# Kernel optimization log

Measured on AMD Instinct MI355X. Metric: run time of the kernel, lower is better.

The kernel has to match this reference:

```python
import jax, jax.numpy as jnp
import numpy as np
from jax import lax

B, H, W, C = 16, 256, 256, 1
LOC_C = 31            # channels out of localization network
BN_EPS = 1e-3         # Keras BatchNormalization default epsilon
NEG_SLOPE = 0.1       # LeakyReLU slope


def _conv_relu(x, k, b):
    y = lax.conv_general_dilated(x, k, (1, 1), 'SAME',
                                 dimension_numbers=('NHWC', 'HWIO', 'NHWC'))
    return jax.nn.relu(y + b)


def _maxpool2(x):
    return lax.reduce_window(x, -jnp.inf, lax.max, (1, 2, 2, 1), (1, 2, 2, 1), 'VALID')


def _resize_nearest(x, out_h, out_w):
    # tf.image.resize(..., method='nearest') with half-pixel centers
    b, h, w, c = x.shape
    ih = jnp.floor((jnp.arange(out_h) + 0.5) * h / out_h).astype(jnp.int32)
    iw = jnp.floor((jnp.arange(out_w) + 0.5) * w / out_w).astype(jnp.int32)
    return x[:, ih][:, :, iw]


def _generate_grid(theta, height, width):
    # base grid in [-1, 1], x varies along width, y along height
    xs = jnp.arange(width, dtype=jnp.float32) / (width - 1) * 2.0 - 1.0
    ys = jnp.arange(height, dtype=jnp.float32) / (height - 1) * 2.0 - 1.0
    gx, gy = jnp.meshgrid(xs, ys)                      # (H, W)
    grid = jnp.stack([gx, gy], axis=-1).reshape(height * width, 2)  # (HW, 2)
    th = theta.reshape(-1, 2, 3)
    A = th[:, :, :2]                                   # (B, 2, 2)
    t = th[:, :, 2]                                    # (B, 2)
    # NOTE: source does grid @ A (not A @ grid) -- replicate exactly
    tg = jnp.einsum('nc,bcd->bnd', grid, A) + t[:, None, :]
    return tg.reshape(-1, height, width, 2)


def _sampler(img, grid):
    b, h, w, c = img.shape
    x = 0.5 * ((grid[..., 0] + 1.0) * (w - 1))
    y = 0.5 * ((grid[..., 1] + 1.0) * (h - 1))
    x0 = jnp.floor(x); x1 = x0 + 1.0
    y0 = jnp.floor(y); y1 = y0 + 1.0
    x0 = jnp.clip(x0, 0.0, w - 1.0); x1 = jnp.clip(x1, 0.0, w - 1.0)
    y0 = jnp.clip(y0, 0.0, h - 1.0); y1 = jnp.clip(y1, 0.0, h - 1.0)
    wa = (x1 - x) * (y1 - y)
    wb = (x1 - x) * (y - y0)
    wc = (x - x0) * (y1 - y)
    wd = (x - x0) * (y - y0)
    xi0 = x0.astype(jnp.int32); xi1 = x1.astype(jnp.int32)
    yi0 = y0.astype(jnp.int32); yi1 = y1.astype(jnp.int32)
    img_flat = img.reshape(b, h * w, c)

    def gather(yi, xi):
        idx = (yi * w + xi).reshape(b, h * w, 1)       # (B, HW, 1)
        return jnp.take_along_axis(img_flat, idx, axis=1).reshape(b, h, w, c)

    Ia = gather(yi0, xi0)
    Ib = gather(yi1, xi0)
    Ic = gather(yi0, xi1)
    Id = gather(yi1, xi1)
    return (wa[..., None] * Ia + wb[..., None] * Ib
            + wc[..., None] * Ic + wd[..., None] * Id)


def setup_inputs() -> dict:
    key = jax.random.key(0)
    ks = jax.random.split(key, 16)
    s = 0.05
    feat = (H // 8) * (W // 8) * LOC_C  # 31744 flattened localization features
    return {
        'x': jax.random.normal(ks[0], (B, H, W, C), jnp.float32),
        'conv1_k': jax.random.normal(ks[1], (3, 3, C, 8), jnp.float32) * s,
        'conv1_b': jnp.zeros((8,), jnp.float32),
        'conv2_k': jax.random.normal(ks[2], (3, 3, 8, 16), jnp.float32) * s,
        'conv2_b': jnp.zeros((16,), jnp.float32),
        'conv3_k': jax.random.normal(ks[3], (3, 3, 16, LOC_C), jnp.float32) * s,
        'conv3_b': jnp.zeros((LOC_C,), jnp.float32),
        'bn_gamma': 1.0 + 0.1 * jax.random.normal(ks[4], (feat,), jnp.float32),
        'bn_beta': 0.1 * jax.random.normal(ks[5], (feat,), jnp.float32),
        'bn_mean': jnp.zeros((feat,), jnp.float32),
        'bn_var': jnp.ones((feat,), jnp.float32),
        'd1_k': jax.random.normal(ks[6], (feat, 64), jnp.float32) * 0.01,
        'd1_b': jnp.zeros((64,), jnp.float32),
        'd2_k': jax.random.normal(ks[7], (64, 96), jnp.float32) * s,
        'd2_b': jnp.zeros((96,), jnp.float32),
        'd3_k': jax.random.normal(ks[8], (96, 6), jnp.float32) * 0.01,
        'd3_b': jnp.array([1, 0, 0, 0, 1, 0], jnp.float32),
    }


def reference(x, conv1_k, conv1_b, conv2_k, conv2_b, conv3_k, conv3_b,
              bn_gamma, bn_beta, bn_mean, bn_var,
              d1_k, d1_b, d2_k, d2_b, d3_k, d3_b):
    # localization network: (conv-relu, pool) x3 -> (B, H/8, W/8, 31)
    xi = _maxpool2(_conv_relu(x, conv1_k, conv1_b))
    xi = _maxpool2(_conv_relu(xi, conv2_k, conv2_b))
    x_intermediate = _maxpool2(_conv_relu(xi, conv3_k, conv3_b))
    # transformation parameter network (BN in inference mode, dropout = identity)
    f = x_intermediate.reshape(x.shape[0], -1)
    f = (f - bn_mean) * jax.lax.rsqrt(bn_var + BN_EPS) * bn_gamma + bn_beta
    f = jax.nn.relu(f @ d1_k + d1_b)
    f = jax.nn.relu(f @ d2_k + d2_b)
    theta = f @ d3_k + d3_b                            # (B, 6)
    grid = _generate_grid(theta, H, W)                 # (B, H, W, 2)
    loc_up = _resize_nearest(x_intermediate, H, W)     # (B, H, W, 31)
    xc = jnp.concatenate([x, loc_up], axis=-1)         # (B, H, W, 32)
    out = _sampler(xc, grid)
    return jnp.where(out >= 0, out, NEG_SLOPE * out)
```

## Files before the change

### kernel.cpp

```cpp
#include <hip/hip_runtime.h>


#define NEG_SLOPE 0.1f
#define BN_EPS 1e-3f

typedef float vfloat4 __attribute__((ext_vector_type(4)));

__device__ __forceinline__ void fma4v(float pv, float4 wq, float* __restrict__ acc) {
    acc[0] = fmaf(pv, wq.x, acc[0]);
    acc[1] = fmaf(pv, wq.y, acc[1]);
    acc[2] = fmaf(pv, wq.z, acc[2]);
    acc[3] = fmaf(pv, wq.w, acc[3]);
}

__global__ __launch_bounds__(256) void st_conv1(const float* __restrict__ x,
                                                const float* __restrict__ w,
                                                const float* __restrict__ bias,
                                                float* __restrict__ Ap,
                                                float* __restrict__ Bp) {
    int idx = blockIdx.x * 256 + threadIdx.x;
    int px = idx & 127, py = (idx >> 7) & 127, b = idx >> 14;
    const float* xb = x + b * 65536;
    int iy0 = 2 * py - 1, ix0 = 2 * px - 1;
    float p[16];
#pragma unroll
    for (int r = 0; r < 4; ++r) {
        int iy = iy0 + r;
        bool oky = (iy >= 0) && (iy < 256);
#pragma unroll
        for (int cc = 0; cc < 4; ++cc) {
            int ix = ix0 + cc;
            bool ok = oky && (ix >= 0) && (ix < 256);
            p[r * 4 + cc] = ok ? xb[iy * 256 + ix] : 0.0f;
        }
    }
    float m[8];
#pragma unroll
    for (int co = 0; co < 8; ++co) m[co] = -1e30f;
#pragma unroll
    for (int oy = 0; oy < 2; ++oy)
#pragma unroll
        for (int ox = 0; ox < 2; ++ox) {
            float acc[8];
#pragma unroll
            for (int co = 0; co < 8; ++co) acc[co] = 0.0f;
#pragma unroll
            for (int ky = 0; ky < 3; ++ky)
#pragma unroll
                for (int kx = 0; kx < 3; ++kx) {
                    float pv = p[(oy + ky) * 4 + (ox + kx)];
                    const float* wr = w + (ky * 3 + kx) * 8;
#pragma unroll
                    for (int co = 0; co < 8; ++co)
                        acc[co] = fmaf(pv, wr[co], acc[co]);
                }
#pragma unroll
            for (int co = 0; co < 8; ++co) m[co] = fmaxf(m[co], acc[co]);
        }
    float4 o0, o1;
    float r0 = m[0] + bias[0], r1 = m[1] + bias[1], r2 = m[2] + bias[2], r3 = m[3] + bias[3];
    float r4 = m[4] + bias[4], r5 = m[5] + bias[5], r6 = m[6] + bias[6], r7 = m[7] + bias[7];
    o0.x = r0 > 0.f ? r0 : 0.f; o0.y = r1 > 0.f ? r1 : 0.f;
    o0.z = r2 > 0.f ? r2 : 0.f; o0.w = r3 > 0.f ? r3 : 0.f;
    o1.x = r4 > 0.f ? r4 : 0.f; o1.y = r5 > 0.f ? r5 : 0.f;
    o1.z = r6 > 0.f ? r6 : 0.f; o1.w = r7 > 0.f ? r7 : 0.f;
    float* o = Ap + ((b * 130 + py + 1) * 130 + (px + 1)) * 8;
    *(float4*)o = o0;
    *(float4*)(o + 4) = o1;

    const float4 z4 = {0.f, 0.f, 0.f, 0.f};
    if (idx < 8256) {
        int bb = idx / 516, t = idx - bb * 516;
        int iy, ix;
        if (t < 130)      { iy = 0;       ix = t; }
        else if (t < 260) { iy = 129;     ix = t - 130; }
        else if (t < 388) { iy = t - 259; ix = 0; }
        else              { iy = t - 387; ix = 129; }
        float* d = Ap + ((bb * 130 + iy) * 130 + ix) * 8;
        *(float4*)d = z4; *(float4*)(d + 4) = z4;
    } else if (idx < 12416) {
        int r = idx - 8256;
        int bb = r / 260, t = r - bb * 260;
        int iy, ix;
        if (t < 66)       { iy = 0;       ix = t; }
        else if (t < 132) { iy = 65;      ix = t - 66; }
        else if (t < 196) { iy = t - 131; ix = 0; }
        else              { iy = t - 195; ix = 65; }
        float* d = Bp + ((bb * 66 + iy) * 66 + ix) * 16;
        *(float4*)d = z4; *(float4*)(d + 4) = z4;
        *(float4*)(d + 8) = z4; *(float4*)(d + 12) = z4;
    }
}

__global__ __launch_bounds__(256) void st_conv2(const float* __restrict__ Ap,
                                                const float* __restrict__ w,
                                                const float* __restrict__ bias,
                                                float* __restrict__ Bp) {
    __shared__ __align__(16) float wlds[1152];
    int t = threadIdx.x;
    for (int i = t; i < 1152; i += 256) wlds[i] = w[i];
    __syncthreads();
    int lane = t & 63;
    int wv = __builtin_amdgcn_readfirstlane(t >> 6);
    int cobase = wv * 4;
    int pixel = blockIdx.x * 64 + lane;
    int px = pixel & 63, py = (pixel >> 6) & 63, b = pixel >> 12;
    const float* Ab = Ap + b * 135200;
    int rowbase = (2 * py) * 130 + 2 * px;
    float acc[4][4];
#pragma unroll
    for (int pos = 0; pos < 4; ++pos)
#pragma unroll
        for (int c = 0; c < 4; ++c) acc[pos][c] = 0.0f;

#pragma unroll
    for (int ciq = 0; ciq < 2; ++ciq) {
        float ps[64];
#pragma unroll
        for (int r = 0; r < 4; ++r)
#pragma unroll
            for (int cc = 0; cc < 4; ++cc) {
                float4 v = *(const float4*)(Ab + (rowbase + r * 130 + cc) * 8 + ciq * 4);
                int cell = r * 4 + cc;
                ps[cell * 4 + 0] = v.x; ps[cell * 4 + 1] = v.y;
                ps[cell * 4 + 2] = v.z; ps[cell * 4 + 3] = v.w;
            }
#pragma unroll
        for (int ky = 0; ky < 3; ++ky)
#pragma unroll
            for (int kx = 0; kx < 3; ++kx) {
                int tap = ky * 3 + kx;
#pragma unroll
                for (int comp = 0; comp < 4; ++comp) {
                    float4 wq = *(const float4*)&wlds[((tap * 8 + ciq * 4 + comp) << 4) + cobase];
#pragma unroll
                    for (int oy = 0; oy < 2; ++oy)
#pragma unroll
                        for (int ox = 0; ox < 2; ++ox) {
                            float pv = ps[((oy + ky) * 4 + (ox + kx)) * 4 + comp];
                            fma4v(pv, wq, acc[oy * 2 + ox]);
                        }
                }
            }
    }
    float4 o;
    float* oc = (float*)&o;
#pragma unroll
    for (int c = 0; c < 4; ++c) {
        float m = fmaxf(fmaxf(acc[0][c], acc[1][c]), fmaxf(acc[2][c], acc[3][c]));
        m += bias[cobase + c];
        oc[c] = m > 0.0f ? m : 0.0f;
    }
    *(float4*)(Bp + ((b * 66 + py + 1) * 66 + (px + 1)) * 16 + cobase) = o;
}

__global__ __launch_bounds__(256) void st_conv3(const float* __restrict__ Bp,
                                                const float* __restrict__ w,
                                                const float* __restrict__ bias,
                                                float* __restrict__ xip) {
    __shared__ __align__(16) float wlds[9 * 16 * 32];
    int t = threadIdx.x;
    for (int i = t; i < 4464; i += 256) {
        int tapci = i / 31;
        int co = i - tapci * 31;
        wlds[(tapci << 5) + co] = w[i];
    }
    __syncthreads();
    int lane = t & 63;
    int wv = __builtin_amdgcn_readfirstlane(t >> 6);
    int quad = blockIdx.y * 4 + wv;
    int cobase = quad * 4;
    if (cobase > 27) cobase = 27;
    int pixel = blockIdx.x * 64 + lane;
    int b = pixel >> 10;
    int cell = pixel & 1023;
    int ppy = cell >> 5, ppx = cell & 31;
    const float* Bb = Bp + b * 69696;
    int rowbase = (2 * ppy) * 66 + 2 * ppx;
    float acc[4][4];
#pragma unroll
    for (int pos = 0; pos < 4; ++pos)
#pragma unroll
        for (int c = 0; c < 4; ++c) acc[pos][c] = 0.0f;

#pragma unroll 2
    for (int ciq = 0; ciq < 4; ++ciq) {
        float ps[64];
#pragma unroll
        for (int r = 0; r < 4; ++r)
#pragma unroll
            for (int cc = 0; cc < 4; ++cc) {
                float4 v = *(const float4*)(Bb + (rowbase + r * 66 + cc) * 16 + ciq * 4);
                int cell2 = r * 4 + cc;
                ps[cell2 * 4 + 0] = v.x; ps[cell2 * 4 + 1] = v.y;
                ps[cell2 * 4 + 2] = v.z; ps[cell2 * 4 + 3] = v.w;
            }
#pragma unroll
        for (int ky = 0; ky < 3; ++ky)
#pragma unroll
            for (int kx = 0; kx < 3; ++kx) {
                int tap = ky * 3 + kx;
#pragma unroll
                for (int comp = 0; comp < 4; ++comp) {
                    float4 wq = *(const float4*)&wlds[((tap * 16 + ciq * 4 + comp) << 5) + cobase];
#pragma unroll
                    for (int oy = 0; oy < 2; ++oy)
#pragma unroll
                        for (int ox = 0; ox < 2; ++ox) {
                            float pv = ps[((oy + ky) * 4 + (ox + kx)) * 4 + comp];
                            fma4v(pv, wq, acc[oy * 2 + ox]);
                        }
                }
            }
    }
    float* xcell = xip + (b << 15) + (cell << 5) + 1 + cobase;
#pragma unroll
    for (int c = 0; c < 4; ++c) {
        float m = fmaxf(fmaxf(acc[0][c], acc[1][c]), fmaxf(acc[2][c], acc[3][c]));
        m += bias[cobase + c];
        xcell[c] = m > 0.0f ? m : 0.0f;
    }
}

__global__ __launch_bounds__(256) void st_d1(const float* __restrict__ xip,
                                             const float* __restrict__ gamma,
                                             const float* __restrict__ beta,
                                             const float* __restrict__ mean,
                                             const float* __restrict__ var,
                                             const float* __restrict__ k1,
                                             float* __restrict__ partial) {
    int t = threadIdx.x, s = blockIdx.x;
    int o = t & 63;
    int sub = t >> 6;
    int subu = __builtin_amdgcn_readfirstlane(sub);
    int j0 = s * 64 + subu * 16;
    float acc[16];
#pragma unroll
    for (int b = 0; b < 16; ++b) acc[b] = 0.0f;
#pragma unroll 4
    for (int jj = 0; jj < 16; ++jj) {
        int j = j0 + jj;
        float kv = k1[j * 64 + o];
        int cell = j / 31;
        int co = j - cell * 31;
        const float* xj = xip + (cell << 5) + 1 + co;
        float sc = gamma[j] * rsqrtf(var[j] + BN_EPS);
        float mn = mean[j], bt = beta[j];
#pragma unroll
        for (int b = 0; b < 16; ++b) {
            float v = xj[b << 15];
            float f = (v - mn) * sc + bt;
            acc[b] = fmaf(f, kv, acc[b]);
        }
    }
    __shared__ float red[4][16][64];
#pragma unroll
    for (int b = 0; b < 16; ++b) red[sub][b][o] = acc[b];
    __syncthreads();
    if (sub == 0) {
#pragma unroll
        for (int b = 0; b < 16; ++b) {
            float v = red[0][b][o] + red[1][b][o] + red[2][b][o] + red[3][b][o];
            partial[b * 31744 + s * 64 + o] = v;
        }
    }
}

__global__ __launch_bounds__(256) void st_head(const float* __restrict__ partial,
                                               const float* __restrict__ b1,
                                               const float* __restrict__ k2,
                                               const float* __restrict__ b2,
                                               const float* __restrict__ k3,
                                               const float* __restrict__ b3,
                                               float* __restrict__ theta) {
    int b = blockIdx.x, t = threadIdx.x;
    __shared__ float red[4][64];
    __shared__ float h1[64];
    __shared__ float h2[96];
    int o = t & 63, qq = t >> 6;
    const float* pb = partial + b * 31744;
    float s = 0.0f;
    int sl0 = qq * 124;
#pragma unroll 4
    for (int sl = sl0; sl < sl0 + 124; ++sl)
        s += pb[sl * 64 + o];
    red[qq][o] = s;
    __syncthreads();
    if (t < 64) {
        float v = red[0][t] + red[1][t] + red[2][t] + red[3][t] + b1[t];
        h1[t] = v > 0.0f ? v : 0.0f;
    }
    __syncthreads();
    if (t < 96) {
        float v = b2[t];
        for (int i = 0; i < 64; ++i) v = fmaf(h1[i], k2[i * 96 + t], v);
        h2[t] = v > 0.0f ? v : 0.0f;
    }
    __syncthreads();
    if (t < 6) {
        float v = b3[t];
        for (int i = 0; i < 96; ++i) v = fmaf(h2[i], k3[i * 6 + t], v);
        theta[b * 6 + t] = v;
    }
}

__global__ __launch_bounds__(256) void st_sample(const float* __restrict__ x,
                                                 const float* __restrict__ xip,
                                                 const float* __restrict__ theta,
                                                 float* __restrict__ out) {
    int gid = blockIdx.x * 256 + threadIdx.x;
    int q = gid & 3;
    int pix = gid >> 2;
    int ow = pix & 255, oh = (pix >> 8) & 255;
    int b = __builtin_amdgcn_readfirstlane(blockIdx.x >> 10);

    const float* th = theta + b * 6;
    float t0 = th[0], t1 = th[1], t2 = th[2], t3 = th[3], t4 = th[4], t5 = th[5];
    float gx = (float)ow * (2.0f / 255.0f) - 1.0f;
    float gy = (float)oh * (2.0f / 255.0f) - 1.0f;
    float sx = gx * t0 + gy * t3 + t2;
    float sy = gx * t1 + gy * t4 + t5;
    float xf = 0.5f * ((sx + 1.0f) * 255.0f);
    float yf = 0.5f * ((sy + 1.0f) * 255.0f);
    float x0 = floorf(xf), y0 = floorf(yf);
    float x1 = x0 + 1.0f, y1 = y0 + 1.0f;
    x0 = fminf(fmaxf(x0, 0.0f), 255.0f);
    x1 = fminf(fmaxf(x1, 0.0f), 255.0f);
    y0 = fminf(fmaxf(y0, 0.0f), 255.0f);
    y1 = fminf(fmaxf(y1, 0.0f), 255.0f);
    float wa = (x1 - xf) * (y1 - yf);
    float wb = (x1 - xf) * (yf - y0);
    float wc = (xf - x0) * (y1 - yf);
    float wd = (xf - x0) * (yf - y0);
    int xi0 = (int)x0, xi1 = (int)x1, yi0 = (int)y0, yi1 = (int)y1;

    const float* cellbase = xip + (b << 15);
    int off = q * 8;
    const float* pa = cellbase + ((((yi0 >> 3) << 5) + (xi0 >> 3)) << 5) + off;
    const float* pb = cellbase + ((((yi1 >> 3) << 5) + (xi0 >> 3)) << 5) + off;
    const float* pc = cellbase + ((((yi0 >> 3) << 5) + (xi1 >> 3)) << 5) + off;
    const float* pd = cellbase + ((((yi1 >> 3) << 5) + (xi1 >> 3)) << 5) + off;

    float r[8];
#pragma unroll
    for (int k = 0; k < 2; ++k) {
        float4 va = *(const float4*)(pa + 4 * k);
        float4 vb = *(const float4*)(pb + 4 * k);
        float4 vc = *(const float4*)(pc + 4 * k);
        float4 vd = *(const float4*)(pd + 4 * k);
        r[4 * k]     = fmaf(wa, va.x, fmaf(wb, vb.x, fmaf(wc, vc.x, wd * vd.x)));
        r[4 * k + 1] = fmaf(wa, va.y, fmaf(wb, vb.y, fmaf(wc, vc.y, wd * vd.y)));
        r[4 * k + 2] = fmaf(wa, va.z, fmaf(wb, vb.z, fmaf(wc, vc.z, wd * vd.z)));
        r[4 * k + 3] = fmaf(wa, va.w, fmaf(wb, vb.w, fmaf(wc, vc.w, wd * vd.w)));
    }
    if (q == 0) {
        const float* xb = x + b * 65536;
        float Ia = xb[yi0 * 256 + xi0];
        float Ib = xb[yi1 * 256 + xi0];
        float Ic = xb[yi0 * 256 + xi1];
        float Id = xb[yi1 * 256 + xi1];
        r[0] = fmaf(wa, Ia, fmaf(wb, Ib, fmaf(wc, Ic, wd * Id)));
    }
#pragma unroll
    for (int i = 0; i < 8; ++i) r[i] = r[i] >= 0.0f ? r[i] : NEG_SLOPE * r[i];

    float* ob = out + pix * 32 + off;
    vfloat4 v0 = {r[0], r[1], r[2], r[3]};
    vfloat4 v1 = {r[4], r[5], r[6], r[7]};
    __builtin_nontemporal_store(v0, (vfloat4*)ob);
    __builtin_nontemporal_store(v1, (vfloat4*)(ob + 4));
}

extern "C" void kernel_launch(void* const* d_in, const int* in_sizes, int n_in,
                              void* d_out, int out_size, void* d_ws, size_t ws_size,
                              hipStream_t stream) {
    const float* x     = (const float*)d_in[0];
    const float* c1k   = (const float*)d_in[1];
    const float* c1b   = (const float*)d_in[2];
    const float* c2k   = (const float*)d_in[3];
    const float* c2b   = (const float*)d_in[4];
    const float* c3k   = (const float*)d_in[5];
    const float* c3b   = (const float*)d_in[6];
    const float* gamma = (const float*)d_in[7];
    const float* beta  = (const float*)d_in[8];
    const float* mean  = (const float*)d_in[9];
    const float* var   = (const float*)d_in[10];
    const float* d1k   = (const float*)d_in[11];
    const float* d1b   = (const float*)d_in[12];
    const float* d2k   = (const float*)d_in[13];
    const float* d2b   = (const float*)d_in[14];
    const float* d3k   = (const float*)d_in[15];
    const float* d3b   = (const float*)d_in[16];
    float* out = (float*)d_out;
    float* ws  = (float*)d_ws;

    float* Ap      = ws;
    float* Bp      = ws + 2163200;
    float* xip     = ws;
    float* partial = ws + 3278336;
    float* theta   = ws + 3786240;

    st_conv1<<<1024, 256, 0, stream>>>(x, c1k, c1b, Ap, Bp);
    st_conv2<<<1024, 256, 0, stream>>>(Ap, c2k, c2b, Bp);
    st_conv3<<<dim3(256, 2), 256, 0, stream>>>(Bp, c3k, c3b, xip);
    st_d1<<<496, 256, 0, stream>>>(xip, gamma, beta, mean, var, d1k, partial);
    st_head<<<16, 256, 0, stream>>>(partial, d1b, d2k, d2b, d3k, d3b, theta);
    st_sample<<<16384, 256, 0, stream>>>(x, xip, theta, out);
}
```

Baseline: 257.1 us.

## Fuse all six stages into one persistent kernel with grid barriers

Replaces the six separate launches (conv1, conv2, conv3, dense-1 partials, head, sampler) with a single persistent kernel of 512 blocks. Stages are separated by a software grid barrier built on an atomic counter and generation word, and each block loops over the work that used to be spread across many blocks. The aim is to remove per-launch overhead and the idle gaps between kernels. In exchange it depends on all 512 blocks being resident at once, which the barrier needs to avoid deadlock, and the sampler runs with fewer blocks looping, which may reduce latency hiding.

```diff
diff --git a/kernel.cpp b/kernel.cpp
--- a/kernel.cpp
+++ b/kernel.cpp
@@ -3,6 +3,7 @@
 
 #define NEG_SLOPE 0.1f
 #define BN_EPS 1e-3f
+#define NBLOCKS 512u
 
 typedef float vfloat4 __attribute__((ext_vector_type(4)));
 
@@ -13,362 +14,382 @@
     acc[3] = fmaf(pv, wq.w, acc[3]);
 }
 
-__global__ __launch_bounds__(256) void st_conv1(const float* __restrict__ x,
-                                                const float* __restrict__ w,
-                                                const float* __restrict__ bias,
-                                                float* __restrict__ Ap,
-                                                float* __restrict__ Bp) {
-    int idx = blockIdx.x * 256 + threadIdx.x;
-    int px = idx & 127, py = (idx >> 7) & 127, b = idx >> 14;
-    const float* xb = x + b * 65536;
-    int iy0 = 2 * py - 1, ix0 = 2 * px - 1;
-    float p[16];
-#pragma unroll
-    for (int r = 0; r < 4; ++r) {
-        int iy = iy0 + r;
-        bool oky = (iy >= 0) && (iy < 256);
-#pragma unroll
-        for (int cc = 0; cc < 4; ++cc) {
-            int ix = ix0 + cc;
-            bool ok = oky && (ix >= 0) && (ix < 256);
-            p[r * 4 + cc] = ok ? xb[iy * 256 + ix] : 0.0f;
-        }
-    }
-    float m[8];
-#pragma unroll
-    for (int co = 0; co < 8; ++co) m[co] = -1e30f;
-#pragma unroll
-    for (int oy = 0; oy < 2; ++oy)
-#pragma unroll
-        for (int ox = 0; ox < 2; ++ox) {
-            float acc[8];
-#pragma unroll
-            for (int co = 0; co < 8; ++co) acc[co] = 0.0f;
+__device__ __forceinline__ void grid_barrier(unsigned* counter, unsigned* gen) {
+    __syncthreads();
+    if (threadIdx.x == 0) {
+        __threadfence();
+        unsigned g = __hip_atomic_load(gen, __ATOMIC_RELAXED, __HIP_MEMORY_SCOPE_AGENT);
+        unsigned arrived = __hip_atomic_fetch_add(counter, 1u, __ATOMIC_ACQ_REL,
+                                                  __HIP_MEMORY_SCOPE_AGENT);
+        if (arrived == NBLOCKS - 1u) {
+            __hip_atomic_store(counter, 0u, __ATOMIC_RELAXED, __HIP_MEMORY_SCOPE_AGENT);
+            __hip_atomic_store(gen, g + 1u, __ATOMIC_RELEASE, __HIP_MEMORY_SCOPE_AGENT);
+        } else {
+            while (__hip_atomic_load(gen, __ATOMIC_ACQUIRE, __HIP_MEMORY_SCOPE_AGENT) == g) {
+                __builtin_amdgcn_s_sleep(8);
+            }
+        }
+        __threadfence();
+    }
+    __syncthreads();
+}
+
+__global__ __launch_bounds__(256, 2) void st_mega(
+    const float* __restrict__ x,
+    const float* __restrict__ c1k, const float* __restrict__ c1b,
+    const float* __restrict__ c2k, const float* __restrict__ c2b,
+    const float* __restrict__ c3k, const float* __restrict__ c3b,
+    const float* __restrict__ gamma, const float* __restrict__ beta,
+    const float* __restrict__ mean, const float* __restrict__ var,
+    const float* __restrict__ d1k, const float* __restrict__ d1b,
+    const float* __restrict__ d2k, const float* __restrict__ d2b,
+    const float* __restrict__ d3k, const float* __restrict__ d3b,
+    float* __restrict__ Ap, float* __restrict__ Bp,
+    float* __restrict__ partial, float* __restrict__ theta,
+    unsigned* __restrict__ barC, unsigned* __restrict__ barG,
+    float* __restrict__ out)
+{
+    __shared__ __align__(16) float smem[4608];
+    const int t = threadIdx.x;
+    const int bid = blockIdx.x;
+    const int gtid = bid * 256 + t;
+    const int lane = t & 63;
+    float* xip = Ap;
+
+#pragma unroll
+    for (int it = 0; it < 2; ++it) {
+        int idx = it * 131072 + gtid;
+        int px = idx & 127, py = (idx >> 7) & 127, b = idx >> 14;
+        const float* xb = x + b * 65536;
+        int iy0 = 2 * py - 1, ix0 = 2 * px - 1;
+        float p[16];
+#pragma unroll
+        for (int r = 0; r < 4; ++r) {
+            int iy = iy0 + r;
+            bool oky = (iy >= 0) && (iy < 256);
+#pragma unroll
+            for (int cc = 0; cc < 4; ++cc) {
+                int ix = ix0 + cc;
+                bool ok = oky && (ix >= 0) && (ix < 256);
+                p[r * 4 + cc] = ok ? xb[iy * 256 + ix] : 0.0f;
+            }
+        }
+        float m[8];
+#pragma unroll
+        for (int co = 0; co < 8; ++co) m[co] = -1e30f;
+#pragma unroll
+        for (int oy = 0; oy < 2; ++oy)
+#pragma unroll
+            for (int ox = 0; ox < 2; ++ox) {
+                float acc[8];
+#pragma unroll
+                for (int co = 0; co < 8; ++co) acc[co] = 0.0f;
+#pragma unroll
+                for (int ky = 0; ky < 3; ++ky)
+#pragma unroll
+                    for (int kx = 0; kx < 3; ++kx) {
+                        float pv = p[(oy + ky) * 4 + (ox + kx)];
+                        const float* wr = c1k + (ky * 3 + kx) * 8;
+#pragma unroll
+                        for (int co = 0; co < 8; ++co)
+                            acc[co] = fmaf(pv, wr[co], acc[co]);
+                    }
+#pragma unroll
+                for (int co = 0; co < 8; ++co) m[co] = fmaxf(m[co], acc[co]);
+            }
+        float4 o0, o1;
+        float r0 = m[0] + c1b[0], r1 = m[1] + c1b[1], r2 = m[2] + c1b[2], r3 = m[3] + c1b[3];
+        float r4 = m[4] + c1b[4], r5 = m[5] + c1b[5], r6 = m[6] + c1b[6], r7 = m[7] + c1b[7];
+        o0.x = r0 > 0.f ? r0 : 0.f; o0.y = r1 > 0.f ? r1 : 0.f;
+        o0.z = r2 > 0.f ? r2 : 0.f; o0.w = r3 > 0.f ? r3 : 0.f;
+        o1.x = r4 > 0.f ? r4 : 0.f; o1.y = r5 > 0.f ? r5 : 0.f;
+        o1.z = r6 > 0.f ? r6 : 0.f; o1.w = r7 > 0.f ? r7 : 0.f;
+        float* o = Ap + ((b * 130 + py + 1) * 130 + (px + 1)) * 8;
+        *(float4*)o = o0;
+        *(float4*)(o + 4) = o1;
+
+        const float4 z4 = {0.f, 0.f, 0.f, 0.f};
+        if (idx < 8256) {
+            int bb = idx / 516, tt = idx - bb * 516;
+            int iy, ix;
+            if (tt < 130)      { iy = 0;        ix = tt; }
+            else if (tt < 260) { iy = 129;      ix = tt - 130; }
+            else if (tt < 388) { iy = tt - 259; ix = 0; }
+            else               { iy = tt - 387; ix = 129; }
+            float* d = Ap + ((bb * 130 + iy) * 130 + ix) * 8;
+            *(float4*)d = z4; *(float4*)(d + 4) = z4;
+        } else if (idx < 12416) {
+            int r = idx - 8256;
+            int bb = r / 260, tt = r - bb * 260;
+            int iy, ix;
+            if (tt < 66)       { iy = 0;        ix = tt; }
+            else if (tt < 132) { iy = 65;       ix = tt - 66; }
+            else if (tt < 196) { iy = tt - 131; ix = 0; }
+            else               { iy = tt - 195; ix = 65; }
+            float* d = Bp + ((bb * 66 + iy) * 66 + ix) * 16;
+            *(float4*)d = z4; *(float4*)(d + 4) = z4;
+            *(float4*)(d + 8) = z4; *(float4*)(d + 12) = z4;
+        }
+    }
+    grid_barrier(barC, barG);
+
+    {
+        for (int i = t; i < 1152; i += 256) smem[i] = c2k[i];
+        __syncthreads();
+        int wv = __builtin_amdgcn_readfirstlane(t >> 6);
+        int cobase = wv * 4;
+#pragma unroll
+        for (int it = 0; it < 2; ++it) {
+            int pixel = (it * 512 + bid) * 64 + lane;
+            int px = pixel & 63, py = (pixel >> 6) & 63, b = pixel >> 12;
+            const float* Ab = Ap + b * 135200;
+            int rowbase = (2 * py) * 130 + 2 * px;
+            float acc[4][4];
+#pragma unroll
+            for (int pos = 0; pos < 4; ++pos)
+#pragma unroll
+                for (int c = 0; c < 4; ++c) acc[pos][c] = 0.0f;
+#pragma unroll
+            for (int ciq = 0; ciq < 2; ++ciq) {
+                float ps[64];
+#pragma unroll
+                for (int r = 0; r < 4; ++r)
+#pragma unroll
+                    for (int cc = 0; cc < 4; ++cc) {
+                        float4 v = *(const float4*)(Ab + (rowbase + r * 130 + cc) * 8 + ciq * 4);
+                        int cell = r * 4 + cc;
+                        ps[cell * 4 + 0] = v.x; ps[cell * 4 + 1] = v.y;
+                        ps[cell * 4 + 2] = v.z; ps[cell * 4 + 3] = v.w;
+                    }
+#pragma unroll
+                for (int ky = 0; ky < 3; ++ky)
+#pragma unroll
+                    for (int kx = 0; kx < 3; ++kx) {
+                        int tap = ky * 3 + kx;
+#pragma unroll
+                        for (int comp = 0; comp < 4; ++comp) {
+                            float4 wq = *(const float4*)&smem[((tap * 8 + ciq * 4 + comp) << 4) + cobase];
+#pragma unroll
+                            for (int oy = 0; oy < 2; ++oy)
+#pragma unroll
+                                for (int ox = 0; ox < 2; ++ox) {
+                                    float pv = ps[((oy + ky) * 4 + (ox + kx)) * 4 + comp];
+                                    fma4v(pv, wq, acc[oy * 2 + ox]);
+                                }
+                        }
+                    }
+            }
+            float4 o;
+            float* oc = (float*)&o;
+#pragma unroll
+            for (int c = 0; c < 4; ++c) {
+                float m = fmaxf(fmaxf(acc[0][c], acc[1][c]), fmaxf(acc[2][c], acc[3][c]));
+                m += c2b[cobase + c];
+                oc[c] = m > 0.0f ? m : 0.0f;
+            }
+            *(float4*)(Bp + ((b * 66 + py + 1) * 66 + (px + 1)) * 16 + cobase) = o;
+        }
+    }
+    grid_barrier(barC, barG);
+
+    {
+        for (int i = t; i < 4464; i += 256) {
+            int tapci = i / 31;
+            int co = i - tapci * 31;
+            smem[(tapci << 5) + co] = c3k[i];
+        }
+        __syncthreads();
+        int wv = __builtin_amdgcn_readfirstlane(t >> 6);
+        int quad = ((bid & 1) << 2) + wv;
+        int cobase = quad * 4;
+        if (cobase > 27) cobase = 27;
+        int pixel = (bid >> 1) * 64 + lane;
+        int b = pixel >> 10;
+        int cell = pixel & 1023;
+        int ppy = cell >> 5, ppx = cell & 31;
+        const float* Bb = Bp + b * 69696;
+        int rowbase = (2 * ppy) * 66 + 2 * ppx;
+        float acc[4][4];
+#pragma unroll
+        for (int pos = 0; pos < 4; ++pos)
+#pragma unroll
+            for (int c = 0; c < 4; ++c) acc[pos][c] = 0.0f;
+#pragma unroll 2
+        for (int ciq = 0; ciq < 4; ++ciq) {
+            float ps[64];
+#pragma unroll
+            for (int r = 0; r < 4; ++r)
+#pragma unroll
+                for (int cc = 0; cc < 4; ++cc) {
+                    float4 v = *(const float4*)(Bb + (rowbase + r * 66 + cc) * 16 + ciq * 4);
+                    int cell2 = r * 4 + cc;
+                    ps[cell2 * 4 + 0] = v.x; ps[cell2 * 4 + 1] = v.y;
+                    ps[cell2 * 4 + 2] = v.z; ps[cell2 * 4 + 3] = v.w;
+                }
 #pragma unroll
             for (int ky = 0; ky < 3; ++ky)
 #pragma unroll
                 for (int kx = 0; kx < 3; ++kx) {
-                    float pv = p[(oy + ky) * 4 + (ox + kx)];
-                    const float* wr = w + (ky * 3 + kx) * 8;
-#pragma unroll
-                    for (int co = 0; co < 8; ++co)
-                        acc[co] = fmaf(pv, wr[co], acc[co]);
+                    int tap = ky * 3 + kx;
+#pragma unroll
+                    for (int comp = 0; comp < 4; ++comp) {
+                        float4 wq = *(const float4*)&smem[((tap * 16 + ciq * 4 + comp) << 5) + cobase];
+#pragma unroll
+                        for (int oy = 0; oy < 2; ++oy)
+#pragma unroll
+                            for (int ox = 0; ox < 2; ++ox) {
+                                float pv = ps[((oy + ky) * 4 + (ox + kx)) * 4 + comp];
+                                fma4v(pv, wq, acc[oy * 2 + ox]);
+                            }
+                    }
                 }
-#pragma unroll
-            for (int co = 0; co < 8; ++co) m[co] = fmaxf(m[co], acc[co]);
-        }
-    float4 o0, o1;
-    float r0 = m[0] + bias[0], r1 = m[1] + bias[1], r2 = m[2] + bias[2], r3 = m[3] + bias[3];
-    float r4 = m[4] + bias[4], r5 = m[5] + bias[5], r6 = m[6] + bias[6], r7 = m[7] + bias[7];
-    o0.x = r0 > 0.f ? r0 : 0.f; o0.y = r1 > 0.f ? r1 : 0.f;
-    o0.z = r2 > 0.f ? r2 : 0.f; o0.w = r3 > 0.f ? r3 : 0.f;
-    o1.x = r4 > 0.f ? r4 : 0.f; o1.y = r5 > 0.f ? r5 : 0.f;
-    o1.z = r6 > 0.f ? r6 : 0.f; o1.w = r7 > 0.f ? r7 : 0.f;
-    float* o = Ap + ((b * 130 + py + 1) * 130 + (px + 1)) * 8;
-    *(float4*)o = o0;
-    *(float4*)(o + 4) = o1;
-
-    const float4 z4 = {0.f, 0.f, 0.f, 0.f};
-    if (idx < 8256) {
-        int bb = idx / 516, t = idx - bb * 516;
-        int iy, ix;
-        if (t < 130)      { iy = 0;       ix = t; }
-        else if (t < 260) { iy = 129;     ix = t - 130; }
-        else if (t < 388) { iy = t - 259; ix = 0; }
-        else              { iy = t - 387; ix = 129; }
-        float* d = Ap + ((bb * 130 + iy) * 130 + ix) * 8;
-        *(float4*)d = z4; *(float4*)(d + 4) = z4;
-    } else if (idx < 12416) {
-        int r = idx - 8256;
-        int bb = r / 260, t = r - bb * 260;
-        int iy, ix;
-        if (t < 66)       { iy = 0;       ix = t; }
-        else if (t < 132) { iy = 65;      ix = t - 66; }
-        else if (t < 196) { iy = t - 131; ix = 0; }
-        else              { iy = t - 195; ix = 65; }
-        float* d = Bp + ((bb * 66 + iy) * 66 + ix) * 16;
-        *(float4*)d = z4; *(float4*)(d + 4) = z4;
-        *(float4*)(d + 8) = z4; *(float4*)(d + 12) = z4;
-    }
-}
-
-__global__ __launch_bounds__(256) void st_conv2(const float* __restrict__ Ap,
-                                                const float* __restrict__ w,
-                                                const float* __restrict__ bias,
-                                                float* __restrict__ Bp) {
-    __shared__ __align__(16) float wlds[1152];
-    int t = threadIdx.x;
-    for (int i = t; i < 1152; i += 256) wlds[i] = w[i];
-    __syncthreads();
-    int lane = t & 63;
-    int wv = __builtin_amdgcn_readfirstlane(t >> 6);
-    int cobase = wv * 4;
-    int pixel = blockIdx.x * 64 + lane;
-    int px = pixel & 63, py = (pixel >> 6) & 63, b = pixel >> 12;
-    const float* Ab = Ap + b * 135200;
-    int rowbase = (2 * py) * 130 + 2 * px;
-    float acc[4][4];
-#pragma unroll
-    for (int pos = 0; pos < 4; ++pos)
-#pragma unroll
-        for (int c = 0; c < 4; ++c) acc[pos][c] = 0.0f;
-
-#pragma unroll
-    for (int ciq = 0; ciq < 2; ++ciq) {
-        float ps[64];
-#pragma unroll
-        for (int r = 0; r < 4; ++r)
-#pragma unroll
-            for (int cc = 0; cc < 4; ++cc) {
-                float4 v = *(const float4*)(Ab + (rowbase + r * 130 + cc) * 8 + ciq * 4);
-                int cell = r * 4 + cc;
-                ps[cell * 4 + 0] = v.x; ps[cell * 4 + 1] = v.y;
-                ps[cell * 4 + 2] = v.z; ps[cell * 4 + 3] = v.w;
-            }
-#pragma unroll
-        for (int ky = 0; ky < 3; ++ky)
-#pragma unroll
-            for (int kx = 0; kx < 3; ++kx) {
-                int tap = ky * 3 + kx;
-#pragma unroll
-                for (int comp = 0; comp < 4; ++comp) {
-                    float4 wq = *(const float4*)&wlds[((tap * 8 + ciq * 4 + comp) << 4) + cobase];
-#pragma unroll
-                    for (int oy = 0; oy < 2; ++oy)
-#pragma unroll
-                        for (int ox = 0; ox < 2; ++ox) {
-                            float pv = ps[((oy + ky) * 4 + (ox + kx)) * 4 + comp];
-                            fma4v(pv, wq, acc[oy * 2 + ox]);
-                        }
-                }
-            }
-    }
-    float4 o;
-    float* oc = (float*)&o;
-#pragma unroll
-    for (int c = 0; c < 4; ++c) {
-        float m = fmaxf(fmaxf(acc[0][c], acc[1][c]), fmaxf(acc[2][c], acc[3][c]));
-        m += bias[cobase + c];
-        oc[c] = m > 0.0f ? m : 0.0f;
-    }
-    *(float4*)(Bp + ((b * 66 + py + 1) * 66 + (px + 1)) * 16 + cobase) = o;
-}
-
-__global__ __launch_bounds__(256) void st_conv3(const float* __restrict__ Bp,
-                                                const float* __restrict__ w,
-                                                const float* __restrict__ bias,
-                                                float* __restrict__ xip) {
-    __shared__ __align__(16) float wlds[9 * 16 * 32];
-    int t = threadIdx.x;
-    for (int i = t; i < 4464; i += 256) {
-        int tapci = i / 31;
-        int co = i - tapci * 31;
-        wlds[(tapci << 5) + co] = w[i];
-    }
-    __syncthreads();
-    int lane = t & 63;
-    int wv = __builtin_amdgcn_readfirstlane(t >> 6);
-    int quad = blockIdx.y * 4 + wv;
-    int cobase = quad * 4;
-    if (cobase > 27) cobase = 27;
-    int pixel = blockIdx.x * 64 + lane;
-    int b = pixel >> 10;
-    int cell = pixel & 1023;
-    int ppy = cell >> 5, ppx = cell & 31;
-    const float* Bb = Bp + b * 69696;
-    int rowbase = (2 * ppy) * 66 + 2 * ppx;
-    float acc[4][4];
-#pragma unroll
-    for (int pos = 0; pos < 4; ++pos)
-#pragma unroll
-        for (int c = 0; c < 4; ++c) acc[pos][c] = 0.0f;
-
-#pragma unroll 2
-    for (int ciq = 0; ciq < 4; ++ciq) {
-        float ps[64];
-#pragma unroll
-        for (int r = 0; r < 4; ++r)
-#pragma unroll
-            for (int cc = 0; cc < 4; ++cc) {
-                float4 v = *(const float4*)(Bb + (rowbase + r * 66 + cc) * 16 + ciq * 4);
-                int cell2 = r * 4 + cc;
-                ps[cell2 * 4 + 0] = v.x; ps[cell2 * 4 + 1] = v.y;
-                ps[cell2 * 4 + 2] = v.z; ps[cell2 * 4 + 3] = v.w;
-            }
-#pragma unroll
-        for (int ky = 0; ky < 3; ++ky)
-#pragma unroll
-            for (int kx = 0; kx < 3; ++kx) {
-                int tap = ky * 3 + kx;
-#pragma unroll
-                for (int comp = 0; comp < 4; ++comp) {
-                    float4 wq = *(const float4*)&wlds[((tap * 16 + ciq * 4 + comp) << 5) + cobase];
-#pragma unroll
-                    for (int oy = 0; oy < 2; ++oy)
-#pragma unroll
-                        for (int ox = 0; ox < 2; ++ox) {
-                            float pv = ps[((oy + ky) * 4 + (ox + kx)) * 4 + comp];
-                            fma4v(pv, wq, acc[oy * 2 + ox]);
-                        }
-                }
-            }
-    }
-    float* xcell = xip + (b << 15) + (cell << 5) + 1 + cobase;
-#pragma unroll
-    for (int c = 0; c < 4; ++c) {
-        float m = fmaxf(fmaxf(acc[0][c], acc[1][c]), fmaxf(acc[2][c], acc[3][c]));
-        m += bias[cobase + c];
-        xcell[c] = m > 0.0f ? m : 0.0f;
-    }
-}
-
-__global__ __launch_bounds__(256) void st_d1(const float* __restrict__ xip,
-                                             const float* __restrict__ gamma,
-                                             const float* __restrict__ beta,
-                                             const float* __restrict__ mean,
-                                             const float* __restrict__ var,
-                                             const float* __restrict__ k1,
-                                             float* __restrict__ partial) {
-    int t = threadIdx.x, s = blockIdx.x;
-    int o = t & 63;
-    int sub = t >> 6;
-    int subu = __builtin_amdgcn_readfirstlane(sub);
-    int j0 = s * 64 + subu * 16;
-    float acc[16];
-#pragma unroll
-    for (int b = 0; b < 16; ++b) acc[b] = 0.0f;
+        }
+        float* xcell = xip + (b << 15) + (cell << 5) + 1 + cobase;
+#pragma unroll
+        for (int c = 0; c < 4; ++c) {
+            float m = fmaxf(fmaxf(acc[0][c], acc[1][c]), fmaxf(acc[2][c], acc[3][c]));
+            m += c3b[cobase + c];
+            xcell[c] = m > 0.0f ? m : 0.0f;
+        }
+    }
+    grid_barrier(barC, barG);
+
+    if (bid < 496) {
+        int s = bid;
+        int o = lane;
+        int sub = t >> 6;
+        int subu = __builtin_amdgcn_readfirstlane(sub);
+        int j0 = s * 64 + subu * 16;
+        float acc[16];
+#pragma unroll
+        for (int b = 0; b < 16; ++b) acc[b] = 0.0f;
 #pragma unroll 4
-    for (int jj = 0; jj < 16; ++jj) {
-        int j = j0 + jj;
-        float kv = k1[j * 64 + o];
-        int cell = j / 31;
-        int co = j - cell * 31;
-        const float* xj = xip + (cell << 5) + 1 + co;
-        float sc = gamma[j] * rsqrtf(var[j] + BN_EPS);
-        float mn = mean[j], bt = beta[j];
-#pragma unroll
-        for (int b = 0; b < 16; ++b) {
-            float v = xj[b << 15];
-            float f = (v - mn) * sc + bt;
-            acc[b] = fmaf(f, kv, acc[b]);
-        }
-    }
-    __shared__ float red[4][16][64];
-#pragma unroll
-    for (int b = 0; b < 16; ++b) red[sub][b][o] = acc[b];
-    __syncthreads();
-    if (sub == 0) {
-#pragma unroll
-        for (int b = 0; b < 16; ++b) {
-            float v = red[0][b][o] + red[1][b][o] + red[2][b][o] + red[3][b][o];
-            partial[b * 31744 + s * 64 + o] = v;
-        }
-    }
-}
-
-__global__ __launch_bounds__(256) void st_head(const float* __restrict__ partial,
-                                               const float* __restrict__ b1,
-                                               const float* __restrict__ k2,
-                                               const float* __restrict__ b2,
-                                               const float* __restrict__ k3,
-                                               const float* __restrict__ b3,
-                                               float* __restrict__ theta) {
-    int b = blockIdx.x, t = threadIdx.x;
-    __shared__ float red[4][64];
-    __shared__ float h1[64];
-    __shared__ float h2[96];
-    int o = t & 63, qq = t >> 6;
-    const float* pb = partial + b * 31744;
-    float s = 0.0f;
-    int sl0 = qq * 124;
+        for (int jj = 0; jj < 16; ++jj) {
+            int j = j0 + jj;
+            float kv = d1k[j * 64 + o];
+            int cell = j / 31;
+            int co = j - cell * 31;
+            const float* xj = xip + (cell << 5) + 1 + co;
+            float sc = gamma[j] * rsqrtf(var[j] + BN_EPS);
+            float mn = mean[j], bt = beta[j];
+#pragma unroll
+            for (int b = 0; b < 16; ++b) {
+                float v = xj[b << 15];
+                float f = (v - mn) * sc + bt;
+                acc[b] = fmaf(f, kv, acc[b]);
+            }
+        }
+        float (*red)[16][64] = (float (*)[16][64])smem;
+#pragma unroll
+        for (int b = 0; b < 16; ++b) red[sub][b][o] = acc[b];
+        __syncthreads();
+        if (sub == 0) {
+#pragma unroll
+            for (int b = 0; b < 16; ++b) {
+                float v = red[0][b][o] + red[1][b][o] + red[2][b][o] + red[3][b][o];
+                partial[b * 31744 + s * 64 + o] = v;
+            }
+        }
+    }
+    grid_barrier(barC, barG);
+
+    if (bid < 16) {
+        int b = bid;
+        float* redh = smem;
+        float* h1   = smem + 256;
+        float* h2   = smem + 320;
+        int o = lane, qq = t >> 6;
+        const float* pb = partial + b * 31744;
+        float s = 0.0f;
+        int sl0 = qq * 124;
 #pragma unroll 4
-    for (int sl = sl0; sl < sl0 + 124; ++sl)
-        s += pb[sl * 64 + o];
-    red[qq][o] = s;
-    __syncthreads();
-    if (t < 64) {
-        float v = red[0][t] + red[1][t] + red[2][t] + red[3][t] + b1[t];
-        h1[t] = v > 0.0f ? v : 0.0f;
-    }
-    __syncthreads();
-    if (t < 96) {
-        float v = b2[t];
-        for (int i = 0; i < 64; ++i) v = fmaf(h1[i], k2[i * 96 + t], v);
-        h2[t] = v > 0.0f ? v : 0.0f;
-    }
-    __syncthreads();
-    if (t < 6) {
-        float v = b3[t];
-        for (int i = 0; i < 96; ++i) v = fmaf(h2[i], k3[i * 6 + t], v);
-        theta[b * 6 + t] = v;
-    }
-}
-
-__global__ __launch_bounds__(256) void st_sample(const float* __restrict__ x,
-                                                 const float* __restrict__ xip,
-                                                 const float* __restrict__ theta,
-                                                 float* __restrict__ out) {
-    int gid = blockIdx.x * 256 + threadIdx.x;
-    int q = gid & 3;
-    int pix = gid >> 2;
-    int ow = pix & 255, oh = (pix >> 8) & 255;
-    int b = __builtin_amdgcn_readfirstlane(blockIdx.x >> 10);
-
-    const float* th = theta + b * 6;
-    float t0 = th[0], t1 = th[1], t2 = th[2], t3 = th[3], t4 = th[4], t5 = th[5];
-    float gx = (float)ow * (2.0f / 255.0f) - 1.0f;
-    float gy = (float)oh * (2.0f / 255.0f) - 1.0f;
-    float sx = gx * t0 + gy * t3 + t2;
-    float sy = gx * t1 + gy * t4 + t5;
-    float xf = 0.5f * ((sx + 1.0f) * 255.0f);
-    float yf = 0.5f * ((sy + 1.0f) * 255.0f);
-    float x0 = floorf(xf), y0 = floorf(yf);
-    float x1 = x0 + 1.0f, y1 = y0 + 1.0f;
-    x0 = fminf(fmaxf(x0, 0.0f), 255.0f);
-    x1 = fminf(fmaxf(x1, 0.0f), 255.0f);
-    y0 = fminf(fmaxf(y0, 0.0f), 255.0f);
-    y1 = fminf(fmaxf(y1, 0.0f), 255.0f);
-    float wa = (x1 - xf) * (y1 - yf);
-    float wb = (x1 - xf) * (yf - y0);
-    float wc = (xf - x0) * (y1 - yf);
-    float wd = (xf - x0) * (yf - y0);
-    int xi0 = (int)x0, xi1 = (int)x1, yi0 = (int)y0, yi1 = (int)y1;
-
-    const float* cellbase = xip + (b << 15);
-    int off = q * 8;
-    const float* pa = cellbase + ((((yi0 >> 3) << 5) + (xi0 >> 3)) << 5) + off;
-    const float* pb = cellbase + ((((yi1 >> 3) << 5) + (xi0 >> 3)) << 5) + off;
-    const float* pc = cellbase + ((((yi0 >> 3) << 5) + (xi1 >> 3)) << 5) + off;
-    const float* pd = cellbase + ((((yi1 >> 3) << 5) + (xi1 >> 3)) << 5) + off;
-
-    float r[8];
-#pragma unroll
-    for (int k = 0; k < 2; ++k) {
-        float4 va = *(const float4*)(pa + 4 * k);
-        float4 vb = *(const float4*)(pb + 4 * k);
-        float4 vc = *(const float4*)(pc + 4 * k);
-        float4 vd = *(const float4*)(pd + 4 * k);
-        r[4 * k]     = fmaf(wa, va.x, fmaf(wb, vb.x, fmaf(wc, vc.x, wd * vd.x)));
-        r[4 * k + 1] = fmaf(wa, va.y, fmaf(wb, vb.y, fmaf(wc, vc.y, wd * vd.y)));
-        r[4 * k + 2] = fmaf(wa, va.z, fmaf(wb, vb.z, fmaf(wc, vc.z, wd * vd.z)));
-        r[4 * k + 3] = fmaf(wa, va.w, fmaf(wb, vb.w, fmaf(wc, vc.w, wd * vd.w)));
-    }
-    if (q == 0) {
-        const float* xb = x + b * 65536;
-        float Ia = xb[yi0 * 256 + xi0];
-        float Ib = xb[yi1 * 256 + xi0];
-        float Ic = xb[yi0 * 256 + xi1];
-        float Id = xb[yi1 * 256 + xi1];
-        r[0] = fmaf(wa, Ia, fmaf(wb, Ib, fmaf(wc, Ic, wd * Id)));
-    }
-#pragma unroll
-    for (int i = 0; i < 8; ++i) r[i] = r[i] >= 0.0f ? r[i] : NEG_SLOPE * r[i];
-
-    float* ob = out + pix * 32 + off;
-    vfloat4 v0 = {r[0], r[1], r[2], r[3]};
-    vfloat4 v1 = {r[4], r[5], r[6], r[7]};
-    __builtin_nontemporal_store(v0, (vfloat4*)ob);
-    __builtin_nontemporal_store(v1, (vfloat4*)(ob + 4));
+        for (int sl = sl0; sl < sl0 + 124; ++sl)
+            s += pb[sl * 64 + o];
+        redh[qq * 64 + o] = s;
+        __syncthreads();
+        if (t < 64) {
+            float v = redh[t] + redh[64 + t] + redh[128 + t] + redh[192 + t] + d1b[t];
+            h1[t] = v > 0.0f ? v : 0.0f;
+        }
+        __syncthreads();
+        if (t < 96) {
+            float v = d2b[t];
+            for (int i = 0; i < 64; ++i) v = fmaf(h1[i], d2k[i * 96 + t], v);
+            h2[t] = v > 0.0f ? v : 0.0f;
+        }
+        __syncthreads();
+        if (t < 6) {
+            float v = d3b[t];
+            for (int i = 0; i < 96; ++i) v = fmaf(h2[i], d3k[i * 6 + t], v);
+            theta[b * 6 + t] = v;
+        }
+    }
+    grid_barrier(barC, barG);
+
+#pragma unroll 1
+    for (int it = 0; it < 32; ++it) {
+        int id = it * 131072 + gtid;
+        int q = id & 3;
+        int pix = id >> 2;
+        int ow = pix & 255, oh = (pix >> 8) & 255;
+        int b = it >> 1;
+
+        const float* th = theta + b * 6;
+        float t0 = th[0], t1 = th[1], t2 = th[2], t3 = th[3], t4 = th[4], t5 = th[5];
+        float gx = (float)ow * (2.0f / 255.0f) - 1.0f;
+        float gy = (float)oh * (2.0f / 255.0f) - 1.0f;
+        float sx = gx * t0 + gy * t3 + t2;
+        float sy = gx * t1 + gy * t4 + t5;
+        float xf = 0.5f * ((sx + 1.0f) * 255.0f);
+        float yf = 0.5f * ((sy + 1.0f) * 255.0f);
+        float x0 = floorf(xf), y0 = floorf(yf);
+        float x1 = x0 + 1.0f, y1 = y0 + 1.0f;
+        x0 = fminf(fmaxf(x0, 0.0f), 255.0f);
+        x1 = fminf(fmaxf(x1, 0.0f), 255.0f);
+        y0 = fminf(fmaxf(y0, 0.0f), 255.0f);
+        y1 = fminf(fmaxf(y1, 0.0f), 255.0f);
+        float wa = (x1 - xf) * (y1 - yf);
+        float wb = (x1 - xf) * (yf - y0);
+        float wc = (xf - x0) * (y1 - yf);
+        float wd = (xf - x0) * (yf - y0);
+        int xi0 = (int)x0, xi1 = (int)x1, yi0 = (int)y0, yi1 = (int)y1;
+
+        const float* cellbase = xip + (b << 15);
+        int off = q * 8;
+        const float* pa = cellbase + ((((yi0 >> 3) << 5) + (xi0 >> 3)) << 5) + off;
+        const float* pbp = cellbase + ((((yi1 >> 3) << 5) + (xi0 >> 3)) << 5) + off;
+        const float* pc = cellbase + ((((yi0 >> 3) << 5) + (xi1 >> 3)) << 5) + off;
+        const float* pd = cellbase + ((((yi1 >> 3) << 5) + (xi1 >> 3)) << 5) + off;
+
+        float r[8];
+#pragma unroll
+        for (int k = 0; k < 2; ++k) {
+            float4 va = *(const float4*)(pa + 4 * k);
+            float4 vb = *(const float4*)(pbp + 4 * k);
+            float4 vc = *(const float4*)(pc + 4 * k);
+            float4 vd = *(const float4*)(pd + 4 * k);
+            r[4 * k]     = fmaf(wa, va.x, fmaf(wb, vb.x, fmaf(wc, vc.x, wd * vd.x)));
+            r[4 * k + 1] = fmaf(wa, va.y, fmaf(wb, vb.y, fmaf(wc, vc.y, wd * vd.y)));
+            r[4 * k + 2] = fmaf(wa, va.z, fmaf(wb, vb.z, fmaf(wc, vc.z, wd * vd.z)));
+            r[4 * k + 3] = fmaf(wa, va.w, fmaf(wb, vb.w, fmaf(wc, vc.w, wd * vd.w)));
+        }
+        if (q == 0) {
+            const float* xb = x + b * 65536;
+            float Ia = xb[yi0 * 256 + xi0];
+            float Ib = xb[yi1 * 256 + xi0];
+            float Ic = xb[yi0 * 256 + xi1];
+            float Id = xb[yi1 * 256 + xi1];
+            r[0] = fmaf(wa, Ia, fmaf(wb, Ib, fmaf(wc, Ic, wd * Id)));
+        }
+#pragma unroll
+        for (int i = 0; i < 8; ++i) r[i] = r[i] >= 0.0f ? r[i] : NEG_SLOPE * r[i];
+
+        float* ob = out + pix * 32 + off;
+        vfloat4 v0 = {r[0], r[1], r[2], r[3]};
+        vfloat4 v1 = {r[4], r[5], r[6], r[7]};
+        __builtin_nontemporal_store(v0, (vfloat4*)ob);
+        __builtin_nontemporal_store(v1, (vfloat4*)(ob + 4));
+    }
 }
 
 extern "C" void kernel_launch(void* const* d_in, const int* in_sizes, int n_in,
@@ -396,14 +417,15 @@
 
     float* Ap      = ws;
     float* Bp      = ws + 2163200;
-    float* xip     = ws;
     float* partial = ws + 3278336;
     float* theta   = ws + 3786240;
-
-    st_conv1<<<1024, 256, 0, stream>>>(x, c1k, c1b, Ap, Bp);
-    st_conv2<<<1024, 256, 0, stream>>>(Ap, c2k, c2b, Bp);
-    st_conv3<<<dim3(256, 2), 256, 0, stream>>>(Bp, c3k, c3b, xip);
-    st_d1<<<496, 256, 0, stream>>>(xip, gamma, beta, mean, var, d1k, partial);
-    st_head<<<16, 256, 0, stream>>>(partial, d1b, d2k, d2b, d3k, d3b, theta);
-    st_sample<<<16384, 256, 0, stream>>>(x, xip, theta, out);
+    unsigned* barC = (unsigned*)(ws + 3786368);
+    unsigned* barG = (unsigned*)(ws + 3786384);
+
+    hipMemsetAsync((void*)barC, 0, 128, stream);
+
+    st_mega<<<NBLOCKS, 256, 0, stream>>>(
+        x, c1k, c1b, c2k, c2b, c3k, c3b, gamma, beta, mean, var,
+        d1k, d1b, d2k, d2b, d3k, d3b, Ap, Bp, partial, theta,
+        barC, barG, out);
 }
```

Result: slower. 924.5 us (+259.5%).

## Fuse conv1 and conv2 into one kernel with conv1 tile in LDS

Applied to the files above, without the earlier changes.

Merges the first conv+pool stage into the second conv kernel. Each block computes the four padded conv1 rows it needs into shared memory, then runs conv2 from LDS instead of a global intermediate buffer. This drops one launch and the global write and read of the 130x130x8 intermediate. In exchange, adjacent blocks recompute the overlapping conv1 halo row, and each block uses about 21 KB of LDS, which may lower occupancy.

```diff
diff --git a/kernel.cpp b/kernel.cpp
--- a/kernel.cpp
+++ b/kernel.cpp
@@ -13,100 +13,81 @@
     acc[3] = fmaf(pv, wq.w, acc[3]);
 }
 
-__global__ __launch_bounds__(256) void st_conv1(const float* __restrict__ x,
-                                                const float* __restrict__ w,
-                                                const float* __restrict__ bias,
-                                                float* __restrict__ Ap,
-                                                float* __restrict__ Bp) {
-    int idx = blockIdx.x * 256 + threadIdx.x;
-    int px = idx & 127, py = (idx >> 7) & 127, b = idx >> 14;
-    const float* xb = x + b * 65536;
-    int iy0 = 2 * py - 1, ix0 = 2 * px - 1;
-    float p[16];
-#pragma unroll
-    for (int r = 0; r < 4; ++r) {
-        int iy = iy0 + r;
-        bool oky = (iy >= 0) && (iy < 256);
-#pragma unroll
-        for (int cc = 0; cc < 4; ++cc) {
-            int ix = ix0 + cc;
-            bool ok = oky && (ix >= 0) && (ix < 256);
-            p[r * 4 + cc] = ok ? xb[iy * 256 + ix] : 0.0f;
-        }
-    }
-    float m[8];
-#pragma unroll
-    for (int co = 0; co < 8; ++co) m[co] = -1e30f;
-#pragma unroll
-    for (int oy = 0; oy < 2; ++oy)
-#pragma unroll
-        for (int ox = 0; ox < 2; ++ox) {
-            float acc[8];
-#pragma unroll
-            for (int co = 0; co < 8; ++co) acc[co] = 0.0f;
-#pragma unroll
-            for (int ky = 0; ky < 3; ++ky)
-#pragma unroll
-                for (int kx = 0; kx < 3; ++kx) {
-                    float pv = p[(oy + ky) * 4 + (ox + kx)];
-                    const float* wr = w + (ky * 3 + kx) * 8;
-#pragma unroll
-                    for (int co = 0; co < 8; ++co)
-                        acc[co] = fmaf(pv, wr[co], acc[co]);
-                }
-#pragma unroll
-            for (int co = 0; co < 8; ++co) m[co] = fmaxf(m[co], acc[co]);
-        }
-    float4 o0, o1;
-    float r0 = m[0] + bias[0], r1 = m[1] + bias[1], r2 = m[2] + bias[2], r3 = m[3] + bias[3];
-    float r4 = m[4] + bias[4], r5 = m[5] + bias[5], r6 = m[6] + bias[6], r7 = m[7] + bias[7];
-    o0.x = r0 > 0.f ? r0 : 0.f; o0.y = r1 > 0.f ? r1 : 0.f;
-    o0.z = r2 > 0.f ? r2 : 0.f; o0.w = r3 > 0.f ? r3 : 0.f;
-    o1.x = r4 > 0.f ? r4 : 0.f; o1.y = r5 > 0.f ? r5 : 0.f;
-    o1.z = r6 > 0.f ? r6 : 0.f; o1.w = r7 > 0.f ? r7 : 0.f;
-    float* o = Ap + ((b * 130 + py + 1) * 130 + (px + 1)) * 8;
-    *(float4*)o = o0;
-    *(float4*)(o + 4) = o1;
-
-    const float4 z4 = {0.f, 0.f, 0.f, 0.f};
-    if (idx < 8256) {
-        int bb = idx / 516, t = idx - bb * 516;
-        int iy, ix;
-        if (t < 130)      { iy = 0;       ix = t; }
-        else if (t < 260) { iy = 129;     ix = t - 130; }
-        else if (t < 388) { iy = t - 259; ix = 0; }
-        else              { iy = t - 387; ix = 129; }
-        float* d = Ap + ((bb * 130 + iy) * 130 + ix) * 8;
-        *(float4*)d = z4; *(float4*)(d + 4) = z4;
-    } else if (idx < 12416) {
-        int r = idx - 8256;
-        int bb = r / 260, t = r - bb * 260;
-        int iy, ix;
-        if (t < 66)       { iy = 0;       ix = t; }
-        else if (t < 132) { iy = 65;      ix = t - 66; }
-        else if (t < 196) { iy = t - 131; ix = 0; }
-        else              { iy = t - 195; ix = 65; }
-        float* d = Bp + ((bb * 66 + iy) * 66 + ix) * 16;
-        *(float4*)d = z4; *(float4*)(d + 4) = z4;
-        *(float4*)(d + 8) = z4; *(float4*)(d + 12) = z4;
-    }
-}
-
-__global__ __launch_bounds__(256) void st_conv2(const float* __restrict__ Ap,
-                                                const float* __restrict__ w,
-                                                const float* __restrict__ bias,
-                                                float* __restrict__ Bp) {
+__global__ __launch_bounds__(256) void st_conv12(const float* __restrict__ x,
+                                                 const float* __restrict__ w1,
+                                                 const float* __restrict__ bias1,
+                                                 const float* __restrict__ w2,
+                                                 const float* __restrict__ bias2,
+                                                 float* __restrict__ Bp) {
+    __shared__ __align__(16) float at[4160];
     __shared__ __align__(16) float wlds[1152];
     int t = threadIdx.x;
-    for (int i = t; i < 1152; i += 256) wlds[i] = w[i];
-    __syncthreads();
+    int blk = blockIdx.x;
+    int b = blk >> 6, py = blk & 63;
+
+    for (int i = t; i < 1152; i += 256) wlds[i] = w2[i];
+    for (int i = t; i < 4160; i += 256) at[i] = 0.0f;
+    __syncthreads();
+
+    const float* xb = x + b * 65536;
+#pragma unroll
+    for (int k = 0; k < 2; ++k) {
+        int p = k * 256 + t;
+        int r = p >> 7;
+        int c = (p & 127) + 1;
+        int ar = 2 * py + r;
+        if (ar >= 1 && ar <= 128) {
+            int pr = ar - 1, pc = c - 1;
+            int iy0 = 2 * pr - 1, ix0 = 2 * pc - 1;
+            float pch[16];
+#pragma unroll
+            for (int rr = 0; rr < 4; ++rr) {
+                int iy = iy0 + rr;
+                bool oky = (iy >= 0) && (iy < 256);
+#pragma unroll
+                for (int cc = 0; cc < 4; ++cc) {
+                    int ix = ix0 + cc;
+                    bool ok = oky && (ix >= 0) && (ix < 256);
+                    pch[rr * 4 + cc] = ok ? xb[iy * 256 + ix] : 0.0f;
+                }
+            }
+            float m[8];
+#pragma unroll
+            for (int co = 0; co < 8; ++co) m[co] = -1e30f;
+#pragma unroll
+            for (int oy = 0; oy < 2; ++oy)
+#pragma unroll
+                for (int ox = 0; ox < 2; ++ox) {
+                    float acc[8];
+#pragma unroll
+                    for (int co = 0; co < 8; ++co) acc[co] = 0.0f;
+#pragma unroll
+                    for (int ky = 0; ky < 3; ++ky)
+#pragma unroll
+                        for (int kx = 0; kx < 3; ++kx) {
+                            float pv = pch[(oy + ky) * 4 + (ox + kx)];
+                            const float* wr = w1 + (ky * 3 + kx) * 8;
+#pragma unroll
+                            for (int co = 0; co < 8; ++co)
+                                acc[co] = fmaf(pv, wr[co], acc[co]);
+                        }
+#pragma unroll
+                    for (int co = 0; co < 8; ++co) m[co] = fmaxf(m[co], acc[co]);
+                }
+            float* dst = &at[(r * 130 + c) * 8];
+#pragma unroll
+            for (int co = 0; co < 8; ++co) {
+                float v = m[co] + bias1[co];
+                dst[co] = v > 0.0f ? v : 0.0f;
+            }
+        }
+    }
+    __syncthreads();
+
     int lane = t & 63;
     int wv = __builtin_amdgcn_readfirstlane(t >> 6);
     int cobase = wv * 4;
-    int pixel = blockIdx.x * 64 + lane;
-    int px = pixel & 63, py = (pixel >> 6) & 63, b = pixel >> 12;
-    const float* Ab = Ap + b * 135200;
-    int rowbase = (2 * py) * 130 + 2 * px;
+    int px = lane;
     float acc[4][4];
 #pragma unroll
     for (int pos = 0; pos < 4; ++pos)
@@ -120,7 +101,7 @@
         for (int r = 0; r < 4; ++r)
 #pragma unroll
             for (int cc = 0; cc < 4; ++cc) {
-                float4 v = *(const float4*)(Ab + (rowbase + r * 130 + cc) * 8 + ciq * 4);
+                float4 v = *(const float4*)&at[((r * 130) + (2 * px + cc)) * 8 + ciq * 4];
                 int cell = r * 4 + cc;
                 ps[cell * 4 + 0] = v.x; ps[cell * 4 + 1] = v.y;
                 ps[cell * 4 + 2] = v.z; ps[cell * 4 + 3] = v.w;
@@ -148,10 +129,24 @@
 #pragma unroll
     for (int c = 0; c < 4; ++c) {
         float m = fmaxf(fmaxf(acc[0][c], acc[1][c]), fmaxf(acc[2][c], acc[3][c]));
-        m += bias[cobase + c];
+        m += bias2[cobase + c];
         oc[c] = m > 0.0f ? m : 0.0f;
     }
     *(float4*)(Bp + ((b * 66 + py + 1) * 66 + (px + 1)) * 16 + cobase) = o;
+
+    int idx = blk * 256 + t;
+    if (idx < 4160) {
+        const float4 z4 = {0.f, 0.f, 0.f, 0.f};
+        int bb = idx / 260, tt = idx - bb * 260;
+        int iy, ix;
+        if (tt < 66)       { iy = 0;        ix = tt; }
+        else if (tt < 132) { iy = 65;       ix = tt - 66; }
+        else if (tt < 196) { iy = tt - 131; ix = 0; }
+        else               { iy = tt - 195; ix = 65; }
+        float* d = Bp + ((bb * 66 + iy) * 66 + ix) * 16;
+        *(float4*)d = z4; *(float4*)(d + 4) = z4;
+        *(float4*)(d + 8) = z4; *(float4*)(d + 12) = z4;
+    }
 }
 
 __global__ __launch_bounds__(256) void st_conv3(const float* __restrict__ Bp,
@@ -394,14 +389,12 @@
     float* out = (float*)d_out;
     float* ws  = (float*)d_ws;
 
-    float* Ap      = ws;
-    float* Bp      = ws + 2163200;
-    float* xip     = ws;
-    float* partial = ws + 3278336;
-    float* theta   = ws + 3786240;
-
-    st_conv1<<<1024, 256, 0, stream>>>(x, c1k, c1b, Ap, Bp);
-    st_conv2<<<1024, 256, 0, stream>>>(Ap, c2k, c2b, Bp);
+    float* Bp      = ws;
+    float* xip     = ws + 1115136;
+    float* partial = ws + 1639424;
+    float* theta   = ws + 2147328;
+
+    st_conv12<<<1024, 256, 0, stream>>>(x, c1k, c1b, c2k, c2b, Bp);
     st_conv3<<<dim3(256, 2), 256, 0, stream>>>(Bp, c3k, c3b, xip);
     st_d1<<<496, 256, 0, stream>>>(xip, gamma, beta, mean, var, d1k, partial);
     st_head<<<16, 256, 0, stream>>>(partial, d1b, d2k, d2b, d3k, d3b, theta);
```

Result: no change. 257.5 us (+0.1%).
